# Performance work log

Measured on AMD Instinct MI355X. Metric: run time of the kernel, lower is better.

The kernel has to match this reference:

```python
import jax, jax.numpy as jnp
import numpy as np

N = 50000        # n nodes (cells)
C = 1024         # common genes
H = 128          # edge_h_dim
HG = 128         # edge_hidden
E = 1600000      # edges (avg degree 32)
LAYERS = 2       # gnn_layers (unset in original __init__; fixed here)
EPS = 1e-8


def setup_inputs() -> dict:
    key = jax.random.key(0)
    ks = jax.random.split(key, 10)
    x_common = jax.random.normal(ks[0], (N, C), dtype=jnp.float32)
    src = jax.random.randint(ks[1], (E,), 0, N, dtype=jnp.int32)
    dst = jax.random.randint(ks[2], (E,), 0, N, dtype=jnp.int32)
    base_w = jax.random.uniform(ks[3], (E,), dtype=jnp.float32)
    # encoder params: Linear(C,H) -> ReLU -> Linear(H,H) -> ReLU
    W1 = jax.random.normal(ks[4], (C, H), dtype=jnp.float32) * 0.02
    b1 = jnp.zeros((H,), dtype=jnp.float32)
    W2 = jax.random.normal(ks[5], (H, H), dtype=jnp.float32) * 0.1
    b2 = jnp.zeros((H,), dtype=jnp.float32)
    # edge gate params: Linear(2H, HG) -> ReLU -> Linear(HG, 1)
    Wg1 = jax.random.normal(ks[6], (2 * H, HG), dtype=jnp.float32) * 0.1
    bg1 = jnp.zeros((HG,), dtype=jnp.float32)
    Wg2 = jax.random.normal(ks[7], (HG, 1), dtype=jnp.float32) * 0.1
    bg2 = jnp.full((1,), 2.0, dtype=jnp.float32)  # original init: bias=2.0
    # node reliability logits
    rho_raw = jax.random.normal(ks[8], (N,), dtype=jnp.float32) * 0.5
    return dict(x_common=x_common, src=src, dst=dst, base_w=base_w,
                W1=W1, b1=b1, W2=W2, b2=b2,
                Wg1=Wg1, bg1=bg1, Wg2=Wg2, bg2=bg2, rho_raw=rho_raw)


def reference(x_common, src, dst, base_w, W1, b1, W2, b2, Wg1, bg1, Wg2, bg2, rho_raw):
    # enc: [N, C] -> [N, H]
    h = jax.nn.relu(jax.nn.relu(x_common @ W1 + b1) @ W2 + b2)
    rho = jax.nn.sigmoid(rho_raw)                 # [N]
    rr = rho[src] * rho[dst]                      # [E] per-edge reliability factor
    for _ in range(LAYERS):
        h_src = h[src]                            # [E, H] gather
        h_dst = h[dst]                            # [E, H] gather
        z = jnp.concatenate([h_src, h_dst], axis=1)               # [E, 2H]
        gate = jax.nn.sigmoid(jax.nn.relu(z @ Wg1 + bg1) @ Wg2 + bg2)[:, 0]  # [E]
        w = base_w * gate * rr                    # [E]
        m = jax.ops.segment_sum(w[:, None] * h_src, dst, num_segments=N)     # [N, H]
        deg = jax.ops.segment_sum(w, dst, num_segments=N)                    # [N]
        h = m / (deg[:, None] + EPS)
    return h
```

## Files before the change

kernel.cpp:

```cpp
#include <hip/hip_runtime.h>
#include <stdint.h>

#define NN 50000
#define CC 1024
#define HH 128
#define EE 1600000
#define EPSV 1e-8f
#define SCAN_BLKS 196

typedef __attribute__((ext_vector_type(8))) short bf16x8;
typedef __attribute__((ext_vector_type(4))) float f32x4;
typedef __attribute__((ext_vector_type(2))) float f32x2;

__device__ __forceinline__ unsigned short f32_to_bf16(float f){
  union { float f; uint32_t u; } cv; cv.f = f;
  uint32_t u = cv.u;
  return (unsigned short)((u + 0x7FFFu + ((u >> 16) & 1u)) >> 16);
}
__device__ __forceinline__ float bf16lo_to_f32(uint32_t w){
  union { uint32_t u; float f; } cv; cv.u = w << 16; return cv.f;
}
__device__ __forceinline__ float bf16hi_to_f32(uint32_t w){
  union { uint32_t u; float f; } cv; cv.u = w & 0xFFFF0000u; return cv.f;
}

#define DPP_ADD(x, ctrl) ((x) + __int_as_float(__builtin_amdgcn_update_dpp(0, __float_as_int(x), (ctrl), 0xF, 0xF, true)))

#define GLOAD_LDS16(g, l) __builtin_amdgcn_global_load_lds( \
    (const __attribute__((address_space(1))) uint32_t*)(g), \
    (__attribute__((address_space(3))) uint32_t*)(l), 16, 0, 0)


__global__ __launch_bounds__(256) void k_prep_all(
    const float* __restrict__ W1, const float* __restrict__ W2,
    const float* __restrict__ Wg1,
    unsigned short* __restrict__ W1T, unsigned short* __restrict__ W2T,
    unsigned short* __restrict__ Wg1T){
  int idx = blockIdx.x*256 + threadIdx.x;
  if(idx < 131072){
    int n = idx >> 10, k = idx & 1023;
    W1T[idx] = f32_to_bf16(W1[k*128 + n]);
  } else if(idx < 131072 + 16384){
    int i = idx - 131072;
    int n = i >> 7, k = i & 127;
    W2T[i] = f32_to_bf16(W2[k*128 + n]);
  } else if(idx < 131072 + 16384 + 32768){
    int i = idx - 131072 - 16384;
    int c = i >> 7, k = i & 127;
    int row = (c < 128) ? k : (128 + k);
    int col = (c < 128) ? c : (c - 128);
    Wg1T[i] = f32_to_bf16(Wg1[row*128 + col]);
  }
}


__global__ __launch_bounds__(256) void k_hist(const int* __restrict__ dst,
                                              int* __restrict__ counts,
                                              int* __restrict__ rank){
  int e = blockIdx.x*256 + threadIdx.x;
  if(e < EE) rank[e] = atomicAdd(&counts[dst[e]], 1);
}

__global__ __launch_bounds__(256) void k_scan1(const int* __restrict__ counts,
    int* __restrict__ lexcl, int* __restrict__ bsum){
  __shared__ int buf[256];
  const int t = threadIdx.x, i = blockIdx.x*256 + t;
  int v = (i < NN) ? counts[i] : 0;
  buf[t] = v;
  __syncthreads();
  for(int off = 1; off < 256; off <<= 1){
    int add = (t >= off) ? buf[t-off] : 0;
    __syncthreads();
    buf[t] += add;
    __syncthreads();
  }
  if(i < NN) lexcl[i] = buf[t] - v;
  if(t == 255) bsum[blockIdx.x] = buf[255];
}

__global__ __launch_bounds__(256) void k_scan2(const int* __restrict__ bsum,
    int* __restrict__ bexcl, int* __restrict__ row_ptr){
  __shared__ int buf[256];
  const int t = threadIdx.x;
  int v = (t < SCAN_BLKS) ? bsum[t] : 0;
  buf[t] = v;
  __syncthreads();
  for(int off = 1; off < 256; off <<= 1){
    int add = (t >= off) ? buf[t-off] : 0;
    __syncthreads();
    buf[t] += add;
    __syncthreads();
  }
  if(t < SCAN_BLKS) bexcl[t] = buf[t] - v;
  if(t == 255) row_ptr[NN] = buf[255];
}

__global__ __launch_bounds__(256) void k_scan3(const int* __restrict__ lexcl,
    const int* __restrict__ bexcl, int* __restrict__ row_ptr){
  const int i = blockIdx.x*256 + threadIdx.x;
  if(i >= NN) return;
  row_ptr[i] = lexcl[i] + bexcl[blockIdx.x];
}

__global__ __launch_bounds__(256) void k_fill(const int* __restrict__ src,
    const int* __restrict__ dst, const float* __restrict__ base_w,
    const float* __restrict__ rho_raw, const int* __restrict__ row_ptr,
    const int* __restrict__ rank, float2* __restrict__ scp){
  int e = blockIdx.x*256 + threadIdx.x;
  if(e >= EE) return;
  int s = src[e], d = dst[e];
  int p = row_ptr[d] + rank[e];
  float rs = 1.f/(1.f + __expf(-rho_raw[s]));
  float rd = 1.f/(1.f + __expf(-rho_raw[d]));
  scp[p] = make_float2(base_w[e]*rs*rd, __int_as_float(s));
}


__global__ __launch_bounds__(256) void k_enc1(
    const float* __restrict__ X, const unsigned short* __restrict__ W1T,
    const float* __restrict__ b1, unsigned short* __restrict__ h1)
{
  __shared__ __attribute__((aligned(16))) float          Af[2][64*32];
  __shared__ __attribute__((aligned(16))) unsigned short Bf[2][128*32];

  const int t = threadIdx.x, w = t >> 6, lane = t & 63;
  const int rowL = lane & 15, kq = lane >> 4;
  const int wm = w >> 1, wn = w & 1;
  const int row0 = blockIdx.x * 64;

  const int a_rl0 = w*16 + (lane >> 3);
  const int a_cl  = lane & 7;
  int agr0 = row0 + a_rl0;     if(agr0 >= NN) agr0 = NN-1;
  int agr1 = row0 + a_rl0 + 8; if(agr1 >= NN) agr1 = NN-1;
  const float* a_src0 = X + (size_t)agr0*1024 + (a_cl ^ (a_rl0 & 7))*4;
  const float* a_src1 = X + (size_t)agr1*1024 + (a_cl ^ ((a_rl0+8) & 7))*4;
  const int b_rl0 = w*32 + (lane >> 2);
  const int b_cl  = lane & 3;
  const int bkey0 = (b_rl0 ^ (b_rl0 >> 2)) & 3;
  const int bkey1 = ((b_rl0+16) ^ ((b_rl0+16) >> 2)) & 3;
  const unsigned short* b_src0 = W1T + (size_t)b_rl0*1024 + (b_cl ^ bkey0)*8;
  const unsigned short* b_src1 = W1T + (size_t)(b_rl0+16)*1024 + (b_cl ^ bkey1)*8;

  #define STAGE(buf, k0)  do{                                              \
    GLOAD_LDS16(a_src0 + (k0), &Af[buf][(w*16    )*32]);                   \
    GLOAD_LDS16(a_src1 + (k0), &Af[buf][(w*16 + 8)*32]);                   \
    GLOAD_LDS16(b_src0 + (k0), &Bf[buf][(w*32     )*32]);                  \
    GLOAD_LDS16(b_src1 + (k0), &Bf[buf][(w*32 + 16)*32]);                  \
  }while(0)

  STAGE(0, 0);
  __syncthreads();

  f32x4 acc[2][4] = {};
  const int arow0 = wm*32 + rowL;
  const int akey  = rowL & 7;
  const int bkeyR = (rowL ^ (rowL >> 2)) & 3;

  int cur = 0;
  for(int step = 0; step < 32; step++){
    if(step < 31) STAGE(cur^1, (step+1)*32);
    bf16x8 af[2];
    #pragma unroll
    for(int mf = 0; mf < 2; mf++){
      const int ar = arow0 + mf*16;
      f32x4 x0 = *(const f32x4*)&Af[cur][ar*32 + (((2*kq  ) ^ akey) << 2)];
      f32x4 x1 = *(const f32x4*)&Af[cur][ar*32 + (((2*kq+1) ^ akey) << 2)];
      union { bf16x8 v; unsigned short s[8]; } pk;
      #pragma unroll
      for(int j = 0; j < 4; j++){ pk.s[j] = f32_to_bf16(x0[j]); pk.s[4+j] = f32_to_bf16(x1[j]); }
      af[mf] = pk.v;
    }
    bf16x8 bfr[4];
    #pragma unroll
    for(int nf = 0; nf < 4; nf++){
      const int br = wn*64 + nf*16 + rowL;
      bfr[nf] = *(const bf16x8*)&Bf[cur][br*32 + ((kq ^ bkeyR) << 3)];
    }
    #pragma unroll
    for(int mf = 0; mf < 2; mf++)
      #pragma unroll
      for(int nf = 0; nf < 4; nf++)
        acc[mf][nf] = __builtin_amdgcn_mfma_f32_16x16x32_bf16(af[mf], bfr[nf], acc[mf][nf], 0, 0, 0);
    __syncthreads();
    cur ^= 1;
  }
  #undef STAGE

  #pragma unroll
  for(int mf = 0; mf < 2; mf++){
    #pragma unroll
    for(int nf = 0; nf < 4; nf++){
      const int col = wn*64 + nf*16 + rowL;
      const float bv = b1[col];
      #pragma unroll
      for(int r = 0; r < 4; r++){
        const int gr = row0 + wm*32 + mf*16 + kq*4 + r;
        if(gr < NN) h1[(size_t)gr*128 + col] = f32_to_bf16(fmaxf(acc[mf][nf][r] + bv, 0.f));
      }
    }
  }
}


__device__ __forceinline__ void uv_phase2(
    const unsigned short* hs, const unsigned short* wgl, int row0, int wave, int lane,
    const float* __restrict__ bg1,
    unsigned short* __restrict__ UH, float* __restrict__ Vf)
{
  const int rowL = lane & 15, kq = lane >> 4;
  const int r = wave*16 + rowL;
  f32x4 acc[16] = {};
  #pragma unroll
  for(int ks = 0; ks < 4; ks++){
    const int kc = ks*4 + kq;
    bf16x8 a = *(const bf16x8*)&hs[r*128 + ((kc ^ (r & 15)) << 3)];
    #pragma unroll
    for(int nt = 0; nt < 16; nt++){
      bf16x8 b = *(const bf16x8*)&wgl[(nt*16 + rowL)*128 + ((kc ^ rowL) << 3)];
      acc[nt] = __builtin_amdgcn_mfma_f32_16x16x32_bf16(a, b, acc[nt], 0, 0, 0);
    }
  }
  #pragma unroll
  for(int nt = 0; nt < 16; nt++){
    const int col = nt*16 + rowL;
    #pragma unroll
    for(int rr = 0; rr < 4; rr++){
      const int gr = row0 + wave*16 + kq*4 + rr;
      if(gr < NN){
        if(col < 128) UH[(size_t)gr*256 + col] = f32_to_bf16(acc[nt][rr]);
        else          Vf[(size_t)gr*128 + col - 128] = acc[nt][rr] + bg1[col - 128];
      }
    }
  }
}


__global__ __launch_bounds__(256) void k_uvA(
    const unsigned short* __restrict__ h1, const unsigned short* __restrict__ W2T,
    const float* __restrict__ b2, const unsigned short* __restrict__ Wg1T,
    const float* __restrict__ bg1, unsigned short* __restrict__ UH,
    float* __restrict__ Vf)
{
  __shared__ __attribute__((aligned(16))) unsigned short hs[64*128];
  __shared__ __attribute__((aligned(16))) unsigned short wgl[256*128];
  const int t = threadIdx.x, wave = t >> 6, lane = t & 63;
  const int rowL = lane & 15, kq = lane >> 4;
  const int row0 = blockIdx.x*64;

  bf16x8 wreg[16];
  #pragma unroll
  for(int i = 0; i < 16; i++)
    wreg[i] = *(const bf16x8*)(Wg1T + (i*256 + t)*8);

  int ar = row0 + wave*16 + rowL; if(ar >= NN) ar = NN-1;
  f32x4 acc[8] = {};
  #pragma unroll
  for(int ks = 0; ks < 4; ks++){
    bf16x8 a = *(const bf16x8*)(h1 + (size_t)ar*128 + ks*32 + kq*8);
    #pragma unroll
    for(int nt = 0; nt < 8; nt++){
      bf16x8 b = *(const bf16x8*)(W2T + (nt*16 + rowL)*128 + ks*32 + kq*8);
      acc[nt] = __builtin_amdgcn_mfma_f32_16x16x32_bf16(a, b, acc[nt], 0, 0, 0);
    }
  }
  #pragma unroll
  for(int nt = 0; nt < 8; nt++){
    const int col = nt*16 + rowL;
    const float bv = b2[col];
    #pragma unroll
    for(int r = 0; r < 4; r++){
      const int rw = wave*16 + kq*4 + r;
      const unsigned short hv = f32_to_bf16(fmaxf(acc[nt][r] + bv, 0.f));
      hs[rw*128 + (((col >> 3) ^ (rw & 15)) << 3) + (col & 7)] = hv;
    }
  }
  #pragma unroll
  for(int i = 0; i < 16; i++){
    const int idx = i*256 + t, row = idx >> 4, c = idx & 15;
    *(bf16x8*)&wgl[row*128 + ((c ^ (row & 15)) << 3)] = wreg[i];
  }
  __syncthreads();
  {
    const int r = t >> 2, gr = row0 + r;
    if(gr < NN){
      #pragma unroll
      for(int j8 = 0; j8 < 4; j8++){
        const int chunk = (t & 3)*4 + j8;
        bf16x8 v = *(const bf16x8*)&hs[r*128 + ((chunk ^ (r & 15)) << 3)];
        *(bf16x8*)&UH[(size_t)gr*256 + 128 + chunk*8] = v;
      }
    }
  }
  uv_phase2(hs, wgl, row0, wave, lane, bg1, UH, Vf);
}


__global__ __launch_bounds__(256) void k_uvB(
    const float* __restrict__ hf, const unsigned short* __restrict__ Wg1T,
    const float* __restrict__ bg1, unsigned short* __restrict__ UH,
    float* __restrict__ Vf)
{
  __shared__ __attribute__((aligned(16))) unsigned short hs[64*128];
  __shared__ __attribute__((aligned(16))) unsigned short wgl[256*128];
  const int t = threadIdx.x, wave = t >> 6, lane = t & 63;
  const int row0 = blockIdx.x*64;

  bf16x8 wreg[16];
  #pragma unroll
  for(int i = 0; i < 16; i++)
    wreg[i] = *(const bf16x8*)(Wg1T + (i*256 + t)*8);

  {
    const int r = t >> 2, gr0 = row0 + r;
    const int gr = (gr0 < NN) ? gr0 : NN-1;
    const float* p = hf + (size_t)gr*128 + (t & 3)*32;
    #pragma unroll
    for(int j8 = 0; j8 < 4; j8++){
      f32x4 v0 = *(const f32x4*)(p + j8*8);
      f32x4 v1 = *(const f32x4*)(p + j8*8 + 4);
      union { bf16x8 v; unsigned short s[8]; } pk;
      #pragma unroll
      for(int j = 0; j < 4; j++){ pk.s[j] = f32_to_bf16(v0[j]); pk.s[4+j] = f32_to_bf16(v1[j]); }
      const int chunk = (t & 3)*4 + j8;
      *(bf16x8*)&hs[r*128 + ((chunk ^ (r & 15)) << 3)] = pk.v;
      if(gr0 < NN) *(bf16x8*)&UH[(size_t)gr0*256 + 128 + chunk*8] = pk.v;
    }
  }
  #pragma unroll
  for(int i = 0; i < 16; i++){
    const int idx = i*256 + t, row = idx >> 4, c = idx & 15;
    *(bf16x8*)&wgl[row*128 + ((c ^ (row & 15)) << 3)] = wreg[i];
  }
  __syncthreads();
  uv_phase2(hs, wgl, row0, wave, lane & 63, bg1, UH, Vf);
}


__global__ __launch_bounds__(256) void k_gate_agg(
    const unsigned short* __restrict__ UH, const float* __restrict__ Vf,
    const int* __restrict__ row_ptr, const float2* __restrict__ scp,
    const float* __restrict__ Wg2, const float* __restrict__ bg2p,
    float* __restrict__ out_f32)
{
  __shared__ float2 ws_s[4][64];
  const int wv = threadIdx.x >> 6, lane = threadIdx.x & 63;
  const int gw = blockIdx.x*4 + wv;
  if(gw >= NN) return;
  const int eq = lane >> 4, li = lane & 15;

  f32x4 va = *(const f32x4*)(Vf + (size_t)gw*128 + li*8);
  f32x4 vb = *(const f32x4*)(Vf + (size_t)gw*128 + li*8 + 4);
  f32x4 wa = *(const f32x4*)(Wg2 + li*8);
  f32x4 wb = *(const f32x4*)(Wg2 + li*8 + 4);
  const float vch[8]  = {va[0],va[1],va[2],va[3],vb[0],vb[1],vb[2],vb[3]};
  const float w2ch[8] = {wa[0],wa[1],wa[2],wa[3],wb[0],wb[1],wb[2],wb[3]};
  const float bg2v = bg2p[0];

  const int beg = row_ptr[gw], end = row_ptr[gw+1];
  float a0 = 0.f, a1 = 0.f, wsum = 0.f;

  for(int base = beg; base < end; base += 64){
    const int nb = min(64, end - base);

    float2 sc_c0, sc_c1; bf16x8 u_c0, u_c1;
    {
      const int i0 = (eq     < nb) ? eq     : 0;
      const int i1 = (4 + eq < nb) ? 4 + eq : 0;
      sc_c0 = scp[base + i0]; sc_c1 = scp[base + i1];
      u_c0 = *(const bf16x8*)&UH[(uint32_t)__float_as_int(sc_c0.y)*256u + li*8];
      u_c1 = *(const bf16x8*)&UH[(uint32_t)__float_as_int(sc_c1.y)*256u + li*8];
    }
    for(int q = 0; q < nb; q += 8){
      float2 sc_n0 = sc_c0, sc_n1 = sc_c1; bf16x8 u_n0 = u_c0, u_n1 = u_c1;
      if(q + 8 < nb){
        const int i0 = (q + 8  + eq < nb) ? q + 8  + eq : 0;
        const int i1 = (q + 12 + eq < nb) ? q + 12 + eq : 0;
        sc_n0 = scp[base + i0]; sc_n1 = scp[base + i1];
        u_n0 = *(const bf16x8*)&UH[(uint32_t)__float_as_int(sc_n0.y)*256u + li*8];
        u_n1 = *(const bf16x8*)&UH[(uint32_t)__float_as_int(sc_n1.y)*256u + li*8];
      }
      {
        union { bf16x8 v; uint32_t u32[4]; } uu; uu.v = u_c0;
        float tacc = 0.f;
        #pragma unroll
        for(int p = 0; p < 4; p++){
          const uint32_t w2b = uu.u32[p];
          tacc += fmaxf(bf16lo_to_f32(w2b) + vch[2*p],   0.f) * w2ch[2*p];
          tacc += fmaxf(bf16hi_to_f32(w2b) + vch[2*p+1], 0.f) * w2ch[2*p+1];
        }
        tacc = DPP_ADD(tacc, 0xB1);
        tacc = DPP_ADD(tacc, 0x4E);
        tacc = DPP_ADD(tacc, 0x141);
        tacc = DPP_ADD(tacc, 0x140);
        const float g = 1.f/(1.f + __expf(-(tacc + bg2v)));
        const int idx = q + eq;
        if(li == 0 && idx < nb) ws_s[wv][idx] = make_float2(sc_c0.x*g, sc_c0.y);
      }
      {
        union { bf16x8 v; uint32_t u32[4]; } uu; uu.v = u_c1;
        float tacc = 0.f;
        #pragma unroll
        for(int p = 0; p < 4; p++){
          const uint32_t w2b = uu.u32[p];
          tacc += fmaxf(bf16lo_to_f32(w2b) + vch[2*p],   0.f) * w2ch[2*p];
          tacc += fmaxf(bf16hi_to_f32(w2b) + vch[2*p+1], 0.f) * w2ch[2*p+1];
        }
        tacc = DPP_ADD(tacc, 0xB1);
        tacc = DPP_ADD(tacc, 0x4E);
        tacc = DPP_ADD(tacc, 0x141);
        tacc = DPP_ADD(tacc, 0x140);
        const float g = 1.f/(1.f + __expf(-(tacc + bg2v)));
        const int idx = q + 4 + eq;
        if(li == 0 && idx < nb) ws_s[wv][idx] = make_float2(sc_c1.x*g, sc_c1.y);
      }
      sc_c0 = sc_n0; sc_c1 = sc_n1; u_c0 = u_n0; u_c1 = u_n1;
    }

    #pragma unroll 8
    for(int j = 0; j < nb; j++){
      const float2 p = ws_s[wv][j];
      const float w  = p.x;
      const uint32_t s = (uint32_t)__float_as_int(p.y);
      const uint32_t hw = *(const uint32_t*)&UH[s*256u + 128u + lane*2];
      a0 += w*bf16lo_to_f32(hw);
      a1 += w*bf16hi_to_f32(hw);
      wsum += w;
    }
  }
  const float inv = 1.f/(wsum + EPSV);
  const size_t o = (size_t)gw*128 + lane*2;
  *(f32x2*)&out_f32[o] = (f32x2){a0*inv, a1*inv};
}


extern "C" void kernel_launch(void* const* d_in, const int* in_sizes, int n_in,
                              void* d_out, int out_size, void* d_ws, size_t ws_size,
                              hipStream_t stream) {
  (void)in_sizes; (void)n_in; (void)out_size; (void)ws_size;
  const float* X      = (const float*)d_in[0];
  const int*   src    = (const int*)d_in[1];
  const int*   dst    = (const int*)d_in[2];
  const float* base_w = (const float*)d_in[3];
  const float* W1     = (const float*)d_in[4];
  const float* b1     = (const float*)d_in[5];
  const float* W2     = (const float*)d_in[6];
  const float* b2     = (const float*)d_in[7];
  const float* Wg1    = (const float*)d_in[8];
  const float* bg1    = (const float*)d_in[9];
  const float* Wg2    = (const float*)d_in[10];
  const float* bg2    = (const float*)d_in[11];
  const float* rho    = (const float*)d_in[12];

  char* ws = (char*)d_ws;
  size_t off = 0;
  auto alloc = [&](size_t bytes)->char*{ char* p = ws + off; off += (bytes + 255) & ~(size_t)255; return p; };
  unsigned short* W1T      = (unsigned short*)alloc((size_t)1024*128*2);
  unsigned short* W2T      = (unsigned short*)alloc((size_t)128*128*2);
  unsigned short* Wg1T     = (unsigned short*)alloc((size_t)256*128*2);
  int*            rank     = (int*)alloc((size_t)EE*4);
  float2*         scp      = (float2*)alloc((size_t)EE*8);
  int*            row_ptr  = (int*)alloc((size_t)(NN+1)*4);
  int*            counts   = (int*)alloc((size_t)NN*4);
  int*            lexcl    = (int*)alloc((size_t)NN*4);
  int*            bsum     = (int*)alloc((size_t)256*4);
  int*            bexcl    = (int*)alloc((size_t)256*4);
  unsigned short* h1       = (unsigned short*)alloc((size_t)NN*128*2);
  unsigned short* UH       = (unsigned short*)alloc((size_t)NN*256*2);
  float*          Vf       = (float*)alloc((size_t)NN*128*4);
  float*          hf_B     = (float*)alloc((size_t)NN*128*4);

  hipMemsetAsync(counts, 0, (size_t)NN*4, stream);
  k_prep_all<<<704, 256, 0, stream>>>(W1, W2, Wg1, W1T, W2T, Wg1T);
  k_hist<<<EE/256, 256, 0, stream>>>(dst, counts, rank);
  k_scan1<<<SCAN_BLKS, 256, 0, stream>>>(counts, lexcl, bsum);
  k_scan2<<<1, 256, 0, stream>>>(bsum, bexcl, row_ptr);
  k_scan3<<<SCAN_BLKS, 256, 0, stream>>>(lexcl, bexcl, row_ptr);
  k_fill<<<EE/256, 256, 0, stream>>>(src, dst, base_w, rho, row_ptr, rank, scp);

  k_enc1<<<782, 256, 0, stream>>>(X, W1T, b1, h1);

  k_uvA<<<782, 256, 0, stream>>>(h1, W2T, b2, Wg1T, bg1, UH, Vf);
  k_gate_agg<<<12500, 256, 0, stream>>>(UH, Vf, row_ptr, scp, Wg2, bg2, hf_B);
  k_uvB<<<782, 256, 0, stream>>>(hf_B, Wg1T, bg1, UH, Vf);
  k_gate_agg<<<12500, 256, 0, stream>>>(UH, Vf, row_ptr, scp, Wg2, bg2, (float*)d_out);
}
```

Before: 490.9 us.

## Pre-convert X to bf16, fuse launches, and pass layer output as bf16

```diff
diff --git a/kernel.cpp b/kernel.cpp
--- a/kernel.cpp
+++ b/kernel.cpp
@@ -7,6 +7,11 @@
 #define EE 1600000
 #define EPSV 1e-8f
 #define SCAN_BLKS 196
+#define ENC_BLKS 782
+#define UV_BLKS 782
+#define EDGE_BLKS (EE/256)
+#define CONV_BLKS 25000
+#define PREP_BLKS 704
 
 typedef __attribute__((ext_vector_type(8))) short bf16x8;
 typedef __attribute__((ext_vector_type(4))) float f32x4;
@@ -31,12 +36,32 @@
     (__attribute__((address_space(3))) uint32_t*)(l), 16, 0, 0)
 
 
-__global__ __launch_bounds__(256) void k_prep_all(
+__global__ __launch_bounds__(256) void k_conv_hist_prep(
+    const float* __restrict__ X, unsigned short* __restrict__ Xb,
+    const int* __restrict__ src, const int* __restrict__ dst,
+    int* __restrict__ counts, int* __restrict__ rank,
     const float* __restrict__ W1, const float* __restrict__ W2,
     const float* __restrict__ Wg1,
     unsigned short* __restrict__ W1T, unsigned short* __restrict__ W2T,
-    unsigned short* __restrict__ Wg1T){
-  int idx = blockIdx.x*256 + threadIdx.x;
+    unsigned short* __restrict__ Wg1T)
+{
+  const int b = blockIdx.x;
+  if(b < CONV_BLKS){
+    const size_t i = ((size_t)b*256 + threadIdx.x)*8;
+    f32x4 v0 = *(const f32x4*)(X + i);
+    f32x4 v1 = *(const f32x4*)(X + i + 4);
+    union { bf16x8 v; unsigned short s[8]; } pk;
+    #pragma unroll
+    for(int j = 0; j < 4; j++){ pk.s[j] = f32_to_bf16(v0[j]); pk.s[4+j] = f32_to_bf16(v1[j]); }
+    *(bf16x8*)(Xb + i) = pk.v;
+    return;
+  }
+  if(b < CONV_BLKS + EDGE_BLKS){
+    int e = (b - CONV_BLKS)*256 + threadIdx.x;
+    if(e < EE) rank[e] = atomicAdd(&counts[dst[e]], 1);
+    return;
+  }
+  int idx = (b - CONV_BLKS - EDGE_BLKS)*256 + threadIdx.x;
   if(idx < 131072){
     int n = idx >> 10, k = idx & 1023;
     W1T[idx] = f32_to_bf16(W1[k*128 + n]);
@@ -54,13 +79,6 @@
 }
 
 
-__global__ __launch_bounds__(256) void k_hist(const int* __restrict__ dst,
-                                              int* __restrict__ counts,
-                                              int* __restrict__ rank){
-  int e = blockIdx.x*256 + threadIdx.x;
-  if(e < EE) rank[e] = atomicAdd(&counts[dst[e]], 1);
-}
-
 __global__ __launch_bounds__(256) void k_scan1(const int* __restrict__ counts,
     int* __restrict__ lexcl, int* __restrict__ bsum){
   __shared__ int buf[256];
@@ -98,42 +116,43 @@
 __global__ __launch_bounds__(256) void k_scan3(const int* __restrict__ lexcl,
     const int* __restrict__ bexcl, int* __restrict__ row_ptr){
   const int i = blockIdx.x*256 + threadIdx.x;
-  if(i >= NN) return;
-  row_ptr[i] = lexcl[i] + bexcl[blockIdx.x];
-}
-
-__global__ __launch_bounds__(256) void k_fill(const int* __restrict__ src,
-    const int* __restrict__ dst, const float* __restrict__ base_w,
-    const float* __restrict__ rho_raw, const int* __restrict__ row_ptr,
-    const int* __restrict__ rank, float2* __restrict__ scp){
-  int e = blockIdx.x*256 + threadIdx.x;
-  if(e >= EE) return;
-  int s = src[e], d = dst[e];
-  int p = row_ptr[d] + rank[e];
-  float rs = 1.f/(1.f + __expf(-rho_raw[s]));
-  float rd = 1.f/(1.f + __expf(-rho_raw[d]));
-  scp[p] = make_float2(base_w[e]*rs*rd, __int_as_float(s));
-}
-
-
-__global__ __launch_bounds__(256) void k_enc1(
-    const float* __restrict__ X, const unsigned short* __restrict__ W1T,
-    const float* __restrict__ b1, unsigned short* __restrict__ h1)
+  if(i < NN) row_ptr[i] = lexcl[i] + bexcl[blockIdx.x];
+}
+
+
+__global__ __launch_bounds__(256) void k_enc1_fill(
+    const unsigned short* __restrict__ Xb, const unsigned short* __restrict__ W1T,
+    const float* __restrict__ b1, unsigned short* __restrict__ h1,
+    const int* __restrict__ src, const int* __restrict__ dst,
+    const float* __restrict__ base_w, const float* __restrict__ rho_raw,
+    const int* __restrict__ row_ptr, const int* __restrict__ rank,
+    float2* __restrict__ scp)
 {
-  __shared__ __attribute__((aligned(16))) float          Af[2][64*32];
+  __shared__ __attribute__((aligned(16))) unsigned short Ab[2][64*32];
   __shared__ __attribute__((aligned(16))) unsigned short Bf[2][128*32];
+
+  if(blockIdx.x >= ENC_BLKS){
+    int e = (blockIdx.x - ENC_BLKS)*256 + threadIdx.x;
+    if(e < EE){
+      int s = src[e], d = dst[e];
+      int p = row_ptr[d] + rank[e];
+      float rs = 1.f/(1.f + __expf(-rho_raw[s]));
+      float rd = 1.f/(1.f + __expf(-rho_raw[d]));
+      scp[p] = make_float2(base_w[e]*rs*rd, __int_as_float(s));
+    }
+    return;
+  }
 
   const int t = threadIdx.x, w = t >> 6, lane = t & 63;
   const int rowL = lane & 15, kq = lane >> 4;
   const int wm = w >> 1, wn = w & 1;
   const int row0 = blockIdx.x * 64;
 
-  const int a_rl0 = w*16 + (lane >> 3);
-  const int a_cl  = lane & 7;
-  int agr0 = row0 + a_rl0;     if(agr0 >= NN) agr0 = NN-1;
-  int agr1 = row0 + a_rl0 + 8; if(agr1 >= NN) agr1 = NN-1;
-  const float* a_src0 = X + (size_t)agr0*1024 + (a_cl ^ (a_rl0 & 7))*4;
-  const float* a_src1 = X + (size_t)agr1*1024 + (a_cl ^ ((a_rl0+8) & 7))*4;
+  const int a_rl  = w*16 + (lane >> 2);
+  const int a_cl  = lane & 3;
+  const int akeyW = (a_rl ^ (a_rl >> 2)) & 3;
+  int agr = row0 + a_rl; if(agr >= NN) agr = NN-1;
+  const unsigned short* a_src = Xb + (size_t)agr*1024 + (a_cl ^ akeyW)*8;
   const int b_rl0 = w*32 + (lane >> 2);
   const int b_cl  = lane & 3;
   const int bkey0 = (b_rl0 ^ (b_rl0 >> 2)) & 3;
@@ -142,48 +161,53 @@
   const unsigned short* b_src1 = W1T + (size_t)(b_rl0+16)*1024 + (b_cl ^ bkey1)*8;
 
   #define STAGE(buf, k0)  do{                                              \
-    GLOAD_LDS16(a_src0 + (k0), &Af[buf][(w*16    )*32]);                   \
-    GLOAD_LDS16(a_src1 + (k0), &Af[buf][(w*16 + 8)*32]);                   \
+    GLOAD_LDS16(a_src  + (k0), &Ab[buf][(w*16)*32]);                       \
     GLOAD_LDS16(b_src0 + (k0), &Bf[buf][(w*32     )*32]);                  \
     GLOAD_LDS16(b_src1 + (k0), &Bf[buf][(w*32 + 16)*32]);                  \
   }while(0)
 
-  STAGE(0, 0);
-  __syncthreads();
-
   f32x4 acc[2][4] = {};
   const int arow0 = wm*32 + rowL;
-  const int akey  = rowL & 7;
-  const int bkeyR = (rowL ^ (rowL >> 2)) & 3;
-
-  int cur = 0;
-  for(int step = 0; step < 32; step++){
-    if(step < 31) STAGE(cur^1, (step+1)*32);
+  const int keyR  = (rowL ^ (rowL >> 2)) & 3;
+
+  auto COMPUTE = [&](const unsigned short* afb, const unsigned short* bfb){
     bf16x8 af[2];
     #pragma unroll
-    for(int mf = 0; mf < 2; mf++){
-      const int ar = arow0 + mf*16;
-      f32x4 x0 = *(const f32x4*)&Af[cur][ar*32 + (((2*kq  ) ^ akey) << 2)];
-      f32x4 x1 = *(const f32x4*)&Af[cur][ar*32 + (((2*kq+1) ^ akey) << 2)];
-      union { bf16x8 v; unsigned short s[8]; } pk;
-      #pragma unroll
-      for(int j = 0; j < 4; j++){ pk.s[j] = f32_to_bf16(x0[j]); pk.s[4+j] = f32_to_bf16(x1[j]); }
-      af[mf] = pk.v;
-    }
+    for(int mf = 0; mf < 2; mf++)
+      af[mf] = *(const bf16x8*)&afb[(arow0 + mf*16)*32 + ((kq ^ keyR) << 3)];
     bf16x8 bfr[4];
     #pragma unroll
     for(int nf = 0; nf < 4; nf++){
       const int br = wn*64 + nf*16 + rowL;
-      bfr[nf] = *(const bf16x8*)&Bf[cur][br*32 + ((kq ^ bkeyR) << 3)];
+      bfr[nf] = *(const bf16x8*)&bfb[br*32 + ((kq ^ keyR) << 3)];
     }
     #pragma unroll
     for(int mf = 0; mf < 2; mf++)
       #pragma unroll
       for(int nf = 0; nf < 4; nf++)
         acc[mf][nf] = __builtin_amdgcn_mfma_f32_16x16x32_bf16(af[mf], bfr[nf], acc[mf][nf], 0, 0, 0);
-    __syncthreads();
-    cur ^= 1;
-  }
+  };
+
+  #define STEP(cbuf, sbuf, sk)  do{                                        \
+    STAGE(sbuf, (sk)*32);                                                  \
+    asm volatile("s_waitcnt vmcnt(3)" ::: "memory");                       \
+    __builtin_amdgcn_s_barrier();                                          \
+    __builtin_amdgcn_sched_barrier(0);                                     \
+    COMPUTE(&Ab[cbuf][0], &Bf[cbuf][0]);                                   \
+    __builtin_amdgcn_s_barrier();                                          \
+  }while(0)
+
+  STAGE(0, 0);
+  for(int tt = 0; tt < 30; tt += 2){
+    STEP(0, 1, tt + 1);
+    STEP(1, 0, tt + 2);
+  }
+  STEP(0, 1, 31);
+  asm volatile("s_waitcnt vmcnt(0)" ::: "memory");
+  __builtin_amdgcn_s_barrier();
+  __builtin_amdgcn_sched_barrier(0);
+  COMPUTE(&Ab[1][0], &Bf[1][0]);
+  #undef STEP
   #undef STAGE
 
   #pragma unroll
@@ -296,9 +320,8 @@
 
 
 __global__ __launch_bounds__(256) void k_uvB(
-    const float* __restrict__ hf, const unsigned short* __restrict__ Wg1T,
-    const float* __restrict__ bg1, unsigned short* __restrict__ UH,
-    float* __restrict__ Vf)
+    const unsigned short* __restrict__ Wg1T, const float* __restrict__ bg1,
+    unsigned short* __restrict__ UH, float* __restrict__ Vf)
 {
   __shared__ __attribute__((aligned(16))) unsigned short hs[64*128];
   __shared__ __attribute__((aligned(16))) unsigned short wgl[256*128];
@@ -313,17 +336,12 @@
   {
     const int r = t >> 2, gr0 = row0 + r;
     const int gr = (gr0 < NN) ? gr0 : NN-1;
-    const float* p = hf + (size_t)gr*128 + (t & 3)*32;
+    const unsigned short* p = UH + (size_t)gr*256 + 128 + (t & 3)*32;
     #pragma unroll
     for(int j8 = 0; j8 < 4; j8++){
-      f32x4 v0 = *(const f32x4*)(p + j8*8);
-      f32x4 v1 = *(const f32x4*)(p + j8*8 + 4);
-      union { bf16x8 v; unsigned short s[8]; } pk;
-      #pragma unroll
-      for(int j = 0; j < 4; j++){ pk.s[j] = f32_to_bf16(v0[j]); pk.s[4+j] = f32_to_bf16(v1[j]); }
+      bf16x8 v = *(const bf16x8*)(p + j8*8);
       const int chunk = (t & 3)*4 + j8;
-      *(bf16x8*)&hs[r*128 + ((chunk ^ (r & 15)) << 3)] = pk.v;
-      if(gr0 < NN) *(bf16x8*)&UH[(size_t)gr0*256 + 128 + chunk*8] = pk.v;
+      *(bf16x8*)&hs[r*128 + ((chunk ^ (r & 15)) << 3)] = v;
     }
   }
   #pragma unroll
@@ -332,7 +350,7 @@
     *(bf16x8*)&wgl[row*128 + ((c ^ (row & 15)) << 3)] = wreg[i];
   }
   __syncthreads();
-  uv_phase2(hs, wgl, row0, wave, lane & 63, bg1, UH, Vf);
+  uv_phase2(hs, wgl, row0, wave, lane, bg1, UH, Vf);
 }
 
 
@@ -340,7 +358,7 @@
     const unsigned short* __restrict__ UH, const float* __restrict__ Vf,
     const int* __restrict__ row_ptr, const float2* __restrict__ scp,
     const float* __restrict__ Wg2, const float* __restrict__ bg2p,
-    float* __restrict__ out_f32)
+    float* __restrict__ out_f32, unsigned short* __restrict__ uh_out)
 {
   __shared__ float2 ws_s[4][64];
   const int wv = threadIdx.x >> 6, lane = threadIdx.x & 63;
@@ -428,8 +446,14 @@
     }
   }
   const float inv = 1.f/(wsum + EPSV);
-  const size_t o = (size_t)gw*128 + lane*2;
-  *(f32x2*)&out_f32[o] = (f32x2){a0*inv, a1*inv};
+  const float r0 = a0*inv, r1 = a1*inv;
+  if(uh_out){
+    const uint32_t packed = (uint32_t)f32_to_bf16(r0) | ((uint32_t)f32_to_bf16(r1) << 16);
+    *(uint32_t*)&uh_out[(size_t)gw*256 + 128 + lane*2] = packed;
+  } else {
+    const size_t o = (size_t)gw*128 + lane*2;
+    *(f32x2*)&out_f32[o] = (f32x2){r0, r1};
+  }
 }
 
 
@@ -465,22 +489,25 @@
   int*            bsum     = (int*)alloc((size_t)256*4);
   int*            bexcl    = (int*)alloc((size_t)256*4);
   unsigned short* h1       = (unsigned short*)alloc((size_t)NN*128*2);
-  unsigned short* UH       = (unsigned short*)alloc((size_t)NN*256*2);
+  unsigned short* UH_A     = (unsigned short*)alloc((size_t)NN*256*2);
+  unsigned short* UH_B     = (unsigned short*)alloc((size_t)NN*256*2);
   float*          Vf       = (float*)alloc((size_t)NN*128*4);
-  float*          hf_B     = (float*)alloc((size_t)NN*128*4);
+  unsigned short* Xb       = (unsigned short*)alloc((size_t)NN*CC*2);
 
   hipMemsetAsync(counts, 0, (size_t)NN*4, stream);
-  k_prep_all<<<704, 256, 0, stream>>>(W1, W2, Wg1, W1T, W2T, Wg1T);
-  k_hist<<<EE/256, 256, 0, stream>>>(dst, counts, rank);
+  k_conv_hist_prep<<<CONV_BLKS + EDGE_BLKS + PREP_BLKS, 256, 0, stream>>>(
+      X, Xb, src, dst, counts, rank, W1, W2, Wg1, W1T, W2T, Wg1T);
+
   k_scan1<<<SCAN_BLKS, 256, 0, stream>>>(counts, lexcl, bsum);
   k_scan2<<<1, 256, 0, stream>>>(bsum, bexcl, row_ptr);
   k_scan3<<<SCAN_BLKS, 256, 0, stream>>>(lexcl, bexcl, row_ptr);
-  k_fill<<<EE/256, 256, 0, stream>>>(src, dst, base_w, rho, row_ptr, rank, scp);
-
-  k_enc1<<<782, 256, 0, stream>>>(X, W1T, b1, h1);
-
-  k_uvA<<<782, 256, 0, stream>>>(h1, W2T, b2, Wg1T, bg1, UH, Vf);
-  k_gate_agg<<<12500, 256, 0, stream>>>(UH, Vf, row_ptr, scp, Wg2, bg2, hf_B);
-  k_uvB<<<782, 256, 0, stream>>>(hf_B, Wg1T, bg1, UH, Vf);
-  k_gate_agg<<<12500, 256, 0, stream>>>(UH, Vf, row_ptr, scp, Wg2, bg2, (float*)d_out);
-}
+
+  k_enc1_fill<<<ENC_BLKS + EDGE_BLKS, 256, 0, stream>>>(
+      Xb, W1T, b1, h1, src, dst, base_w, rho, row_ptr, rank, scp);
+
+  k_uvA<<<UV_BLKS, 256, 0, stream>>>(h1, W2T, b2, Wg1T, bg1, UH_A, Vf);
+
+  k_gate_agg<<<12500, 256, 0, stream>>>(UH_A, Vf, row_ptr, scp, Wg2, bg2, nullptr, UH_B);
+  k_uvB<<<UV_BLKS, 256, 0, stream>>>(Wg1T, bg1, UH_B, Vf);
+  k_gate_agg<<<12500, 256, 0, stream>>>(UH_B, Vf, row_ptr, scp, Wg2, bg2, (float*)d_out, nullptr);
+}
```

New measurement: 493.2 us. Within noise of the previous version (+0.5%).
